# Kernel optimization log

Hardware: AMD Instinct MI355X
Metric: run time of the kernel (lower is better)

The kernel has to match this reference:

```python
import jax, jax.numpy as jnp
import numpy as np


def setup_inputs() -> dict:
    key = jax.random.key(0)
    k1, k2, k3 = jax.random.split(key, 3)
    B, L, C, D, V = 8, 512, 4000, 512, 10000
    x = jax.random.uniform(k1, (B, L, C), dtype=jnp.float32)            # dense char n-gram features
    W_proj = jax.random.normal(k2, (D, C), dtype=jnp.float32) * 0.02     # Linear(char_vsize, d_vec), no bias
    emb_matrix = jax.random.uniform(k3, (V, D), dtype=jnp.float32,
                                    minval=-0.1, maxval=0.1)             # QueryEmb latent embedding table
    return {"x": x, "W_proj": W_proj, "emb_matrix": emb_matrix}


def reference(x, W_proj, emb_matrix):
    # charEmbedder: tanh(Linear(x)) per sentence -> vectorized over batch
    q = jnp.tanh(jnp.einsum('blc,dc->bld', x, W_proj))                   # [B, L, D]
    # QueryEmb: softmax(q @ E^T) @ E + q  (dropout in eval mode = identity)
    attn = jax.nn.softmax(jnp.einsum('bld,vd->blv', q, emb_matrix), axis=-1)  # [B, L, V]
    ctx = jnp.einsum('blv,vd->bld', attn, emb_matrix) + q                # residual
    return ctx
```

## Files before the change

### kernel.cpp

```cpp
#include <hip/hip_runtime.h>
#include <hip/hip_bf16.h>

typedef unsigned short u16;
typedef unsigned int u32;
typedef __bf16 bf16x8 __attribute__((ext_vector_type(8)));
typedef u16 u16x8 __attribute__((ext_vector_type(8)));
typedef float f32x4 __attribute__((ext_vector_type(4)));

#define MM   4096
#define CC   4000
#define KP   4096
#define DD   512
#define VV   10000
#define VPAD 10240

#define WS_Q    0u
#define WS_EB   4194304u
#define WS_ET   14680064u
#define WS_LACC 25165824u
#define WS_P    25182208u
#define OFF_XB  0u
#define OFF_WB  33554432u
#define OFF_QA  37748736u
#define FAST_NEED (WS_P + OFF_QA + 16777216u)
#define WS_PACC 109068288u
#define FULLP_NEED (WS_PACC + 67108864u)

__device__ __forceinline__ u16 f2bf(float f) {
  u32 u = __builtin_bit_cast(u32, f);
  return (u16)((u + 0x7FFFu + ((u >> 16) & 1u)) >> 16);
}
__device__ __forceinline__ float bf2f(u16 h) {
  u32 u = (u32)h << 16;
  return __builtin_bit_cast(float, u);
}

#define GLDS(gp, lp) __builtin_amdgcn_global_load_lds( \
    (const __attribute__((address_space(1))) void*)(gp), \
    (__attribute__((address_space(3))) void*)(lp), 16, 0, 0)

__global__ __launch_bounds__(256) void k_eprep(const float* __restrict__ E,
                                               u16* __restrict__ Eb,
                                               u16* __restrict__ ETb,
                                               float* __restrict__ Out,
                                               float* __restrict__ Lacc) {
  __shared__ u16 st[64 * 65];
  int tid = threadIdx.x;
  {
    int bid = blockIdx.x * 8 + blockIdx.y;
    f32x4 z = {0.f, 0.f, 0.f, 0.f};
    #pragma unroll
    for (int rep = 0; rep < 2; ++rep) {
      int id = bid * 256 + tid + rep * 327680;
      if (id < 524288)      *(f32x4*)(Out + (size_t)id * 4) = z;
      else if (id < 525312) *(f32x4*)(Lacc + (size_t)(id - 524288) * 4) = z;
    }
  }
  int v0 = blockIdx.x * 64, d0 = blockIdx.y * 64;
  int r = tid >> 2, seg = tid & 3;
  u16 h[16];
  int v = v0 + r;
  if (v < VV) {
    const float* src = E + (size_t)v * DD + d0 + seg * 16;
    #pragma unroll
    for (int j = 0; j < 4; ++j) {
      float4 t = *(const float4*)(src + j * 4);
      h[4*j+0] = f2bf(t.x); h[4*j+1] = f2bf(t.y); h[4*j+2] = f2bf(t.z); h[4*j+3] = f2bf(t.w);
    }
  } else {
    #pragma unroll
    for (int j = 0; j < 16; ++j) h[j] = 0;
  }
  {
    u16x8 p0, p1;
    #pragma unroll
    for (int j = 0; j < 8; ++j) { p0[j] = h[j]; p1[j] = h[8+j]; }
    u16* dst = Eb + (size_t)v * DD + d0 + seg * 16;
    *(u16x8*)dst = p0; *(u16x8*)(dst + 8) = p1;
  }
  #pragma unroll
  for (int j = 0; j < 16; ++j) st[r * 65 + seg * 16 + j] = h[j];
  __syncthreads();
  {
    u16 g[16];
    #pragma unroll
    for (int j = 0; j < 16; ++j) g[j] = st[(seg * 16 + j) * 65 + r];
    u16x8 p0, p1;
    #pragma unroll
    for (int j = 0; j < 8; ++j) { p0[j] = g[j]; p1[j] = g[8+j]; }
    u16* dst = ETb + (size_t)(d0 + r) * VPAD + v0 + seg * 16;
    *(u16x8*)dst = p0; *(u16x8*)(dst + 8) = p1;
  }
}

__global__ __launch_bounds__(256) void k_conv(const float* __restrict__ X,
                                              const float* __restrict__ Wp,
                                              u16* __restrict__ Xb,
                                              u16* __restrict__ Wb) {
  int row = blockIdx.x;
  int t = threadIdx.x;
  const float* src;
  u16* dst;
  if (row < MM) { src = X + (size_t)row * CC; dst = Xb + (size_t)row * KP; }
  else { src = Wp + (size_t)(row - MM) * CC; dst = Wb + (size_t)(row - MM) * KP; }
  int c0 = t * 16;
  u16 h[16];
  if (c0 + 16 <= CC) {
    #pragma unroll
    for (int j = 0; j < 4; ++j) {
      float4 v = *(const float4*)(src + c0 + j * 4);
      h[4*j+0] = f2bf(v.x); h[4*j+1] = f2bf(v.y); h[4*j+2] = f2bf(v.z); h[4*j+3] = f2bf(v.w);
    }
  } else {
    #pragma unroll
    for (int j = 0; j < 16; ++j) h[j] = 0;
  }
  u16x8 p0, p1;
  #pragma unroll
  for (int j = 0; j < 8; ++j) { p0[j] = h[j]; p1[j] = h[8+j]; }
  *(u16x8*)(dst + c0) = p0; *(u16x8*)(dst + c0 + 8) = p1;
}

__global__ __launch_bounds__(256) void k_g1(const u16* __restrict__ Xb,
                                            const u16* __restrict__ Wb,
                                            float* __restrict__ Qacc) {
  __shared__ u16 As[128 * 64];
  __shared__ u16 Bs[64 * 64];
  int tid = threadIdx.x;
  int m0 = blockIdx.x * 128;
  int n0 = blockIdx.y * 64;
  int kt0 = blockIdx.z * 32;
  int w = tid >> 6, l = tid & 63;
  int l15 = l & 15, quad = l >> 4;
  int lr = l >> 3, lg = l & 7;
  f32x4 acc[2][4] = {};

  for (int kt = kt0; kt < kt0 + 32; ++kt) {
    #pragma unroll
    for (int i = 0; i < 4; ++i) {
      int wc = i * 4 + w;
      int row = wc * 8 + lr;
      int g = lg ^ (row & 7);
      GLDS(Xb + (size_t)(m0 + row) * KP + kt * 64 + g * 8, As + wc * 512);
      if (i < 2)
        GLDS(Wb + (size_t)(n0 + row) * KP + kt * 64 + g * 8, Bs + wc * 512);
    }
    __syncthreads();
    #pragma unroll
    for (int kk = 0; kk < 2; ++kk) {
      bf16x8 a[2], b[4];
      #pragma unroll
      for (int mi = 0; mi < 2; ++mi) {
        int arow = w * 32 + mi * 16 + l15;
        int slot = (kk * 4 + quad) ^ (arow & 7);
        a[mi] = *(const bf16x8*)&As[arow * 64 + slot * 8];
      }
      #pragma unroll
      for (int ni = 0; ni < 4; ++ni) {
        int brow = ni * 16 + l15;
        int slot = (kk * 4 + quad) ^ (brow & 7);
        b[ni] = *(const bf16x8*)&Bs[brow * 64 + slot * 8];
      }
      #pragma unroll
      for (int mi = 0; mi < 2; ++mi)
        #pragma unroll
        for (int ni = 0; ni < 4; ++ni)
          acc[mi][ni] = __builtin_amdgcn_mfma_f32_16x16x32_bf16(a[mi], b[ni], acc[mi][ni], 0, 0, 0);
    }
    __syncthreads();
  }
  float* dst = Qacc + (size_t)blockIdx.z * (MM * DD);
  #pragma unroll
  for (int mi = 0; mi < 2; ++mi)
    #pragma unroll
    for (int ni = 0; ni < 4; ++ni)
      #pragma unroll
      for (int r = 0; r < 4; ++r) {
        int m = m0 + w * 32 + mi * 16 + quad * 4 + r;
        int d = n0 + ni * 16 + l15;
        dst[(size_t)m * DD + d] = acc[mi][ni][r];
      }
}

__global__ __launch_bounds__(256) void k_tanh(const float* __restrict__ Qacc,
                                              u16* __restrict__ Qb) {
  int idx = blockIdx.x * 256 + threadIdx.x;
  size_t base = (size_t)idx * 8;
  f32x4 a0 = *(const f32x4*)(Qacc + base);
  f32x4 a1 = *(const f32x4*)(Qacc + base + 4);
  f32x4 b0 = *(const f32x4*)(Qacc + (size_t)MM * DD + base);
  f32x4 b1 = *(const f32x4*)(Qacc + (size_t)MM * DD + base + 4);
  u16x8 p;
  #pragma unroll
  for (int j = 0; j < 4; ++j) p[j] = f2bf(tanhf(a0[j] + b0[j]));
  #pragma unroll
  for (int j = 0; j < 4; ++j) p[4 + j] = f2bf(tanhf(a1[j] + b1[j]));
  *(u16x8*)(Qb + base) = p;
}

__global__ __launch_bounds__(256) void k_gemm1(const float* __restrict__ X,
                                               const float* __restrict__ W,
                                               u16* __restrict__ Qb) {
  __shared__ u16 xs[64 * 64];
  __shared__ u16 wst[64 * 64];
  int tid = threadIdx.x;
  int m0 = blockIdx.x * 64;
  int n0 = blockIdx.y * 64;
  int srow = tid >> 2;
  int sseg = tid & 3;
  int r7 = srow & 7;
  const float* xsrc = X + (size_t)(m0 + srow) * CC + sseg * 16;
  const float* wsrc = W + (size_t)(n0 + srow) * CC + sseg * 16;
  int lane = tid & 63;
  int wv = tid >> 6;
  int l15 = lane & 15, quad = lane >> 4;
  f32x4 acc[4] = {};

  for (int kt = 0; kt < 63; ++kt) {
    int cbase = kt * 64 + sseg * 16;
    float xv[16], wf[16];
    if (cbase + 16 <= CC) {
      #pragma unroll
      for (int j = 0; j < 4; ++j) {
        float4 tx = *(const float4*)(xsrc + kt * 64 + j * 4);
        float4 tw = *(const float4*)(wsrc + kt * 64 + j * 4);
        xv[4*j+0] = tx.x; xv[4*j+1] = tx.y; xv[4*j+2] = tx.z; xv[4*j+3] = tx.w;
        wf[4*j+0] = tw.x; wf[4*j+1] = tw.y; wf[4*j+2] = tw.z; wf[4*j+3] = tw.w;
      }
    } else {
      #pragma unroll
      for (int j = 0; j < 16; ++j) { xv[j] = 0.f; wf[j] = 0.f; }
    }
    __syncthreads();
    #pragma unroll
    for (int j = 0; j < 2; ++j) {
      int g = (sseg * 2 + j) ^ r7;
      u16x8 px, pw;
      #pragma unroll
      for (int e = 0; e < 8; ++e) { px[e] = f2bf(xv[8*j+e]); pw[e] = f2bf(wf[8*j+e]); }
      *(u16x8*)&xs[srow * 64 + (g << 3)] = px;
      *(u16x8*)&wst[srow * 64 + (g << 3)] = pw;
    }
    __syncthreads();
    #pragma unroll
    for (int kk = 0; kk < 2; ++kk) {
      int arow = 16 * wv + l15;
      int ga = (kk * 4 + quad) ^ (arow & 7);
      bf16x8 a = *(const bf16x8*)&xs[arow * 64 + (ga << 3)];
      #pragma unroll
      for (int nb = 0; nb < 4; ++nb) {
        int brow = 16 * nb + l15;
        int gb = (kk * 4 + quad) ^ (brow & 7);
        bf16x8 b = *(const bf16x8*)&wst[brow * 64 + (gb << 3)];
        acc[nb] = __builtin_amdgcn_mfma_f32_16x16x32_bf16(a, b, acc[nb], 0, 0, 0);
      }
    }
  }
  #pragma unroll
  for (int nb = 0; nb < 4; ++nb) {
    int d = n0 + 16 * nb + l15;
    #pragma unroll
    for (int r = 0; r < 4; ++r) {
      int m = m0 + 16 * wv + 4 * quad + r;
      Qb[(size_t)m * DD + d] = f2bf(tanhf(acc[nb][r]));
    }
  }
}

__global__ __launch_bounds__(256, 4) void k_s(const u16* __restrict__ Qb,
                                              const u16* __restrict__ Eb,
                                              u16* __restrict__ Pg,
                                              float* __restrict__ Lacc,
                                              int cbase, int W) {
  __shared__ u16 S[16384];
  u16* As = S;
  u16* Bs = S + 8192;
  int tid = threadIdx.x;
  int m0 = blockIdx.x * 128;
  int n0 = blockIdx.y * 128;
  int w = tid >> 6, l = tid & 63;
  int l15 = l & 15, quad = l >> 4;
  int mhalf = w >> 1, nhalf = w & 1;
  int lr = l >> 3, lg = l & 7;
  f32x4 acc[4][4] = {};

  for (int kt = 0; kt < 8; ++kt) {
    #pragma unroll
    for (int i = 0; i < 4; ++i) {
      int wc = i * 4 + w;
      int row = wc * 8 + lr;
      int g = lg ^ (row & 7);
      GLDS(Qb + (size_t)(m0 + row) * DD + kt * 64 + g * 8, As + wc * 512);
      GLDS(Eb + (size_t)(cbase + n0 + row) * DD + kt * 64 + g * 8, Bs + wc * 512);
    }
    __syncthreads();
    #pragma unroll
    for (int kk = 0; kk < 2; ++kk) {
      bf16x8 a[4], b[4];
      #pragma unroll
      for (int mi = 0; mi < 4; ++mi) {
        int arow = mhalf * 64 + mi * 16 + l15;
        int slot = (kk * 4 + quad) ^ (arow & 7);
        a[mi] = *(const bf16x8*)&As[arow * 64 + slot * 8];
      }
      #pragma unroll
      for (int ni = 0; ni < 4; ++ni) {
        int brow = nhalf * 64 + ni * 16 + l15;
        int slot = (kk * 4 + quad) ^ (brow & 7);
        b[ni] = *(const bf16x8*)&Bs[brow * 64 + slot * 8];
      }
      #pragma unroll
      for (int mi = 0; mi < 4; ++mi)
        #pragma unroll
        for (int ni = 0; ni < 4; ++ni)
          acc[mi][ni] = __builtin_amdgcn_mfma_f32_16x16x32_bf16(a[mi], b[ni], acc[mi][ni], 0, 0, 0);
    }
    __syncthreads();
  }

  float rs[4][4] = {};
  #pragma unroll
  for (int mi = 0; mi < 4; ++mi) {
    #pragma unroll
    for (int ni = 0; ni < 4; ++ni) {
      int colL = nhalf * 64 + ni * 16 + l15;
      bool ok = (cbase + n0 + colL) < VV;
      #pragma unroll
      for (int r = 0; r < 4; ++r) {
        int rowL = mhalf * 64 + mi * 16 + quad * 4 + r;
        float p = ok ? __expf(acc[mi][ni][r]) : 0.f;
        rs[mi][r] += p;
        S[rowL * 128 + (((colL >> 3) ^ (rowL & 15)) << 3) + (colL & 7)] = f2bf(p);
      }
    }
  }
  __syncthreads();
  {
    int row = tid >> 1, h2 = tid & 1;
    size_t gbase = (size_t)(m0 + row) * W + n0 + h2 * 64;
    #pragma unroll
    for (int g = 0; g < 8; ++g) {
      int pg = (h2 * 8 + g) ^ (row & 15);
      u16x8 v = *(const u16x8*)&S[row * 128 + pg * 8];
      *(u16x8*)(Pg + gbase + g * 8) = v;
    }
  }
  #pragma unroll
  for (int mi = 0; mi < 4; ++mi)
    #pragma unroll
    for (int r = 0; r < 4; ++r) {
      float v = rs[mi][r];
      v += __shfl_xor(v, 1, 16);
      v += __shfl_xor(v, 2, 16);
      v += __shfl_xor(v, 4, 16);
      v += __shfl_xor(v, 8, 16);
      if (l15 == 0)
        atomicAdd(&Lacc[m0 + mhalf * 64 + mi * 16 + quad * 4 + r], v);
    }
}

__global__ __launch_bounds__(256, 4) void k_pvs(const u16* __restrict__ Pg,
                                                const u16* __restrict__ ETb,
                                                float* __restrict__ Pacc) {
  __shared__ u16 S[16384];
  u16* As = S;
  u16* Bs = S + 8192;
  int tid = threadIdx.x;
  int m0 = blockIdx.x * 128;
  int d0 = blockIdx.y * 128;
  int z = blockIdx.z;
  int w = tid >> 6, l = tid & 63;
  int l15 = l & 15, quad = l >> 4;
  int mhalf = w >> 1, nhalf = w & 1;
  int lr = l >> 3, lg = l & 7;
  f32x4 acc[4][4] = {};
  int kt0 = z * 20;

  for (int kt = kt0; kt < kt0 + 20; ++kt) {
    #pragma unroll
    for (int i = 0; i < 4; ++i) {
      int wc = i * 4 + w;
      int row = wc * 8 + lr;
      int g = lg ^ (row & 7);
      GLDS(Pg + (size_t)(m0 + row) * VPAD + kt * 64 + g * 8, As + wc * 512);
      GLDS(ETb + (size_t)(d0 + row) * VPAD + kt * 64 + g * 8, Bs + wc * 512);
    }
    __syncthreads();
    #pragma unroll
    for (int kk = 0; kk < 2; ++kk) {
      bf16x8 a[4], b[4];
      #pragma unroll
      for (int mi = 0; mi < 4; ++mi) {
        int arow = mhalf * 64 + mi * 16 + l15;
        int slot = (kk * 4 + quad) ^ (arow & 7);
        a[mi] = *(const bf16x8*)&As[arow * 64 + slot * 8];
      }
      #pragma unroll
      for (int ni = 0; ni < 4; ++ni) {
        int brow = nhalf * 64 + ni * 16 + l15;
        int slot = (kk * 4 + quad) ^ (brow & 7);
        b[ni] = *(const bf16x8*)&Bs[brow * 64 + slot * 8];
      }
      #pragma unroll
      for (int mi = 0; mi < 4; ++mi)
        #pragma unroll
        for (int ni = 0; ni < 4; ++ni)
          acc[mi][ni] = __builtin_amdgcn_mfma_f32_16x16x32_bf16(a[mi], b[ni], acc[mi][ni], 0, 0, 0);
    }
    __syncthreads();
  }
  float* dst = Pacc + (size_t)z * (MM * DD);
  #pragma unroll
  for (int mi = 0; mi < 4; ++mi)
    #pragma unroll
    for (int ni = 0; ni < 4; ++ni)
      #pragma unroll
      for (int r = 0; r < 4; ++r) {
        int m = m0 + mhalf * 64 + mi * 16 + quad * 4 + r;
        int d = d0 + nhalf * 64 + ni * 16 + l15;
        dst[(size_t)m * DD + d] = acc[mi][ni][r];
      }
}

__global__ __launch_bounds__(256) void k_pv(const u16* __restrict__ Pg,
                                            const u16* __restrict__ ETb,
                                            float* __restrict__ Out,
                                            int cbase, int W) {
  __shared__ u16 As[128 * 64];
  __shared__ u16 Bs[64 * 64];
  int tid = threadIdx.x;
  int m0 = blockIdx.x * 128;
  int n0 = blockIdx.y * 64;
  int w = tid >> 6, l = tid & 63;
  int l15 = l & 15, quad = l >> 4;
  int lr = l >> 3, lg = l & 7;
  int iters = W >> 6;
  f32x4 acc[2][4] = {};

  for (int kt = 0; kt < iters; ++kt) {
    #pragma unroll
    for (int i = 0; i < 4; ++i) {
      int wc = i * 4 + w;
      int row = wc * 8 + lr;
      int g = lg ^ (row & 7);
      GLDS(Pg + (size_t)(m0 + row) * W + kt * 64 + g * 8, As + wc * 512);
      if (i < 2)
        GLDS(ETb + (size_t)(n0 + row) * VPAD + cbase + kt * 64 + g * 8, Bs + wc * 512);
    }
    __syncthreads();
    #pragma unroll
    for (int kk = 0; kk < 2; ++kk) {
      bf16x8 a[2], b[4];
      #pragma unroll
      for (int mi = 0; mi < 2; ++mi) {
        int arow = w * 32 + mi * 16 + l15;
        int slot = (kk * 4 + quad) ^ (arow & 7);
        a[mi] = *(const bf16x8*)&As[arow * 64 + slot * 8];
      }
      #pragma unroll
      for (int ni = 0; ni < 4; ++ni) {
        int brow = ni * 16 + l15;
        int slot = (kk * 4 + quad) ^ (brow & 7);
        b[ni] = *(const bf16x8*)&Bs[brow * 64 + slot * 8];
      }
      #pragma unroll
      for (int mi = 0; mi < 2; ++mi)
        #pragma unroll
        for (int ni = 0; ni < 4; ++ni)
          acc[mi][ni] = __builtin_amdgcn_mfma_f32_16x16x32_bf16(a[mi], b[ni], acc[mi][ni], 0, 0, 0);
    }
    __syncthreads();
  }
  #pragma unroll
  for (int mi = 0; mi < 2; ++mi)
    #pragma unroll
    for (int ni = 0; ni < 4; ++ni)
      #pragma unroll
      for (int r = 0; r < 4; ++r) {
        int m = m0 + w * 32 + mi * 16 + quad * 4 + r;
        int d = n0 + ni * 16 + l15;
        Out[(size_t)m * DD + d] += acc[mi][ni][r];
      }
}

__global__ __launch_bounds__(256) void k_fin8(float* __restrict__ Out,
                                              const float* __restrict__ Lacc,
                                              const u16* __restrict__ Qb,
                                              const float* __restrict__ Pacc) {
  int idx = blockIdx.x * 256 + threadIdx.x;
  int m = idx >> 7;
  int d4 = (idx & 127) * 4;
  float inv = 1.f / Lacc[m];
  size_t off = (size_t)m * DD + d4;
  f32x4 s = {0.f, 0.f, 0.f, 0.f};
  #pragma unroll
  for (int z = 0; z < 8; ++z)
    s += *(const f32x4*)(Pacc + (size_t)z * (MM * DD) + off);
  const u16* qp = Qb + off;
  f32x4 r;
  #pragma unroll
  for (int i = 0; i < 4; ++i) r[i] = s[i] * inv + bf2f(qp[i]);
  *(f32x4*)(Out + off) = r;
}

__global__ __launch_bounds__(256) void k_fin(float* __restrict__ Out,
                                             const float* __restrict__ Lacc,
                                             const u16* __restrict__ Qb) {
  int idx = blockIdx.x * 256 + threadIdx.x;
  int m = idx >> 7;
  int d4 = (idx & 127) * 4;
  float inv = 1.f / Lacc[m];
  f32x4 ov = *(const f32x4*)(Out + (size_t)m * DD + d4);
  const u16* qp = Qb + (size_t)m * DD + d4;
  f32x4 r;
  #pragma unroll
  for (int i = 0; i < 4; ++i) r[i] = ov[i] * inv + bf2f(qp[i]);
  *(f32x4*)(Out + (size_t)m * DD + d4) = r;
}

extern "C" void kernel_launch(void* const* d_in, const int* in_sizes, int n_in,
                              void* d_out, int out_size, void* d_ws, size_t ws_size,
                              hipStream_t stream) {
  const float* x  = (const float*)d_in[0];
  const float* Wp = (const float*)d_in[1];
  const float* E  = (const float*)d_in[2];
  float* out = (float*)d_out;
  char* ws = (char*)d_ws;
  u16*   Qb   = (u16*)(ws + WS_Q);
  u16*   Eb   = (u16*)(ws + WS_EB);
  u16*   ETb  = (u16*)(ws + WS_ET);
  float* Lacc = (float*)(ws + WS_LACC);
  u16*   Pc   = (u16*)(ws + WS_P);
  u16*   Xb   = (u16*)(ws + WS_P + OFF_XB);
  u16*   Wb   = (u16*)(ws + WS_P + OFF_WB);
  float* Qacc = (float*)(ws + WS_P + OFF_QA);
  float* Pacc = (float*)(ws + WS_PACC);

  bool fastg = ws_size >= (size_t)FAST_NEED;
  bool fullp = ws_size >= (size_t)FULLP_NEED;

  k_eprep<<<dim3(VPAD / 64, DD / 64), 256, 0, stream>>>(E, Eb, ETb, out, Lacc);
  if (fastg) {
    k_conv<<<dim3(MM + DD), 256, 0, stream>>>(x, Wp, Xb, Wb);
    k_g1<<<dim3(MM / 128, DD / 64, 2), 256, 0, stream>>>(Xb, Wb, Qacc);
    k_tanh<<<dim3(MM * DD / 8 / 256), 256, 0, stream>>>(Qacc, Qb);
  } else {
    k_gemm1<<<dim3(MM / 64, DD / 64), 256, 0, stream>>>(x, Wp, Qb);
  }
  if (fullp) {
    k_s  <<<dim3(MM / 128, VPAD / 128), 256, 0, stream>>>(Qb, Eb, Pc, Lacc, 0, VPAD);
    k_pvs<<<dim3(MM / 128, DD / 128, 8), 256, 0, stream>>>(Pc, ETb, Pacc);
    k_fin8<<<dim3(MM * DD / 4 / 256), 256, 0, stream>>>(out, Lacc, Qb, Pacc);
  } else {
    int W = 640;
    if (ws_size >= (size_t)WS_P + (size_t)MM * 2560 * 2) W = 2560;
    else if (ws_size >= (size_t)WS_P + (size_t)MM * 1280 * 2) W = 1280;
    int nch = VPAD / W;
    for (int c = 0; c < nch; ++c) {
      k_s <<<dim3(MM / 128, W / 128), 256, 0, stream>>>(Qb, Eb, Pc, Lacc, c * W, W);
      k_pv<<<dim3(MM / 128, DD / 64), 256, 0, stream>>>(Pc, ETb, out, c * W, W);
    }
    k_fin<<<dim3(MM * DD / 4 / 256), 256, 0, stream>>>(out, Lacc, Qb);
  }
}
```

Before: 297.8 us.

## Switch attention GEMMs to FP8 with scaled operands and rebalance split-K

Quantizes the embedding table, its transpose, tanh(q) and the softmax probabilities to FP8 (E4M3-like, with power-of-two prescales) and runs both attention GEMMs on fp8 MFMA instructions. The goal is to halve operand bytes and use the higher fp8 matrix throughput. The projection GEMM moves to 4-way split-K and the PV GEMM to 4-way split, with new tanh and finalize kernels to match. In exchange it loses precision, clamps logits before exp, drops the output zeroing, and adds a workspace-size-gated path.

```diff
diff --git a/kernel.cpp b/kernel.cpp
--- a/kernel.cpp
+++ b/kernel.cpp
@@ -3,9 +3,11 @@
 
 typedef unsigned short u16;
 typedef unsigned int u32;
+typedef unsigned char u8;
 typedef __bf16 bf16x8 __attribute__((ext_vector_type(8)));
 typedef u16 u16x8 __attribute__((ext_vector_type(8)));
 typedef float f32x4 __attribute__((ext_vector_type(4)));
+typedef u32 u32x4 __attribute__((ext_vector_type(4)));
 
 #define MM   4096
 #define CC   4000
@@ -14,17 +16,23 @@
 #define VV   10000
 #define VPAD 10240
 
+#define WS8_QB   0u
+#define WS8_QF   4194304u
+#define WS8_EF   6291456u
+#define WS8_ETF  11534336u
+#define WS8_LACC 16777216u
+#define WS8_R    16793600u
+#define R_XB     0u
+#define R_WB     33554432u
+#define R_QA     37748736u
+#define WS8_PACC 88096768u
+#define FAST8_NEED 121651200u
+
 #define WS_Q    0u
 #define WS_EB   4194304u
 #define WS_ET   14680064u
 #define WS_LACC 25165824u
 #define WS_P    25182208u
-#define OFF_XB  0u
-#define OFF_WB  33554432u
-#define OFF_QA  37748736u
-#define FAST_NEED (WS_P + OFF_QA + 16777216u)
-#define WS_PACC 109068288u
-#define FULLP_NEED (WS_PACC + 67108864u)
 
 __device__ __forceinline__ u16 f2bf(float f) {
   u32 u = __builtin_bit_cast(u32, f);
@@ -34,62 +42,70 @@
   u32 u = (u32)h << 16;
   return __builtin_bit_cast(float, u);
 }
+__device__ __forceinline__ u8 f2fp8(float f) {
+  u32 u = __builtin_bit_cast(u32, f);
+  u32 s = (u >> 31) << 7;
+  u32 m = u & 0x7FFFFFFFu;
+  if (m < 0x3C800000u) return (u8)s;
+  u32 r = m + 0x7FFFFu + ((m >> 20) & 1u);
+  return (u8)(((r >> 20) - 960u) | s);
+}
 
 #define GLDS(gp, lp) __builtin_amdgcn_global_load_lds( \
     (const __attribute__((address_space(1))) void*)(gp), \
     (__attribute__((address_space(3))) void*)(lp), 16, 0, 0)
 
-__global__ __launch_bounds__(256) void k_eprep(const float* __restrict__ E,
-                                               u16* __restrict__ Eb,
-                                               u16* __restrict__ ETb,
-                                               float* __restrict__ Out,
-                                               float* __restrict__ Lacc) {
-  __shared__ u16 st[64 * 65];
+__device__ __forceinline__ int fo8(int row, int o) {
+  return row * 64 + ((((o >> 1) ^ ((row >> 1) & 3)) << 4) | ((o & 1) << 3));
+}
+
+
+__global__ __launch_bounds__(256) void k_eprep8(const float* __restrict__ E,
+                                                u8* __restrict__ Ef,
+                                                u8* __restrict__ ETf,
+                                                float* __restrict__ Lacc) {
+  __shared__ u8 st[64 * 68];
   int tid = threadIdx.x;
   {
-    int bid = blockIdx.x * 8 + blockIdx.y;
-    f32x4 z = {0.f, 0.f, 0.f, 0.f};
-    #pragma unroll
-    for (int rep = 0; rep < 2; ++rep) {
-      int id = bid * 256 + tid + rep * 327680;
-      if (id < 524288)      *(f32x4*)(Out + (size_t)id * 4) = z;
-      else if (id < 525312) *(f32x4*)(Lacc + (size_t)(id - 524288) * 4) = z;
-    }
+    int flat = blockIdx.x * 8 + blockIdx.y;
+    int fid = flat * 256 + tid;
+    if (fid < MM) Lacc[fid] = 0.f;
   }
   int v0 = blockIdx.x * 64, d0 = blockIdx.y * 64;
   int r = tid >> 2, seg = tid & 3;
-  u16 h[16];
+  u8 h[16];
   int v = v0 + r;
   if (v < VV) {
     const float* src = E + (size_t)v * DD + d0 + seg * 16;
     #pragma unroll
     for (int j = 0; j < 4; ++j) {
       float4 t = *(const float4*)(src + j * 4);
-      h[4*j+0] = f2bf(t.x); h[4*j+1] = f2bf(t.y); h[4*j+2] = f2bf(t.z); h[4*j+3] = f2bf(t.w);
+      h[4*j+0] = f2fp8(t.x * 16.f); h[4*j+1] = f2fp8(t.y * 16.f);
+      h[4*j+2] = f2fp8(t.z * 16.f); h[4*j+3] = f2fp8(t.w * 16.f);
     }
   } else {
     #pragma unroll
     for (int j = 0; j < 16; ++j) h[j] = 0;
   }
   {
-    u16x8 p0, p1;
-    #pragma unroll
-    for (int j = 0; j < 8; ++j) { p0[j] = h[j]; p1[j] = h[8+j]; }
-    u16* dst = Eb + (size_t)v * DD + d0 + seg * 16;
-    *(u16x8*)dst = p0; *(u16x8*)(dst + 8) = p1;
-  }
-  #pragma unroll
-  for (int j = 0; j < 16; ++j) st[r * 65 + seg * 16 + j] = h[j];
+    u32x4 p;
+    #pragma unroll
+    for (int q = 0; q < 4; ++q)
+      p[q] = (u32)h[4*q] | ((u32)h[4*q+1] << 8) | ((u32)h[4*q+2] << 16) | ((u32)h[4*q+3] << 24);
+    *(u32x4*)(Ef + (size_t)v * DD + d0 + seg * 16) = p;
+  }
+  #pragma unroll
+  for (int j = 0; j < 16; ++j) st[r * 68 + seg * 16 + j] = h[j];
   __syncthreads();
   {
-    u16 g[16];
-    #pragma unroll
-    for (int j = 0; j < 16; ++j) g[j] = st[(seg * 16 + j) * 65 + r];
-    u16x8 p0, p1;
-    #pragma unroll
-    for (int j = 0; j < 8; ++j) { p0[j] = g[j]; p1[j] = g[8+j]; }
-    u16* dst = ETb + (size_t)(d0 + r) * VPAD + v0 + seg * 16;
-    *(u16x8*)dst = p0; *(u16x8*)(dst + 8) = p1;
+    u8 g[16];
+    #pragma unroll
+    for (int j = 0; j < 16; ++j) g[j] = st[(seg * 16 + j) * 68 + r];
+    u32x4 p;
+    #pragma unroll
+    for (int q = 0; q < 4; ++q)
+      p[q] = (u32)g[4*q] | ((u32)g[4*q+1] << 8) | ((u32)g[4*q+2] << 16) | ((u32)g[4*q+3] << 24);
+    *(u32x4*)(ETf + (size_t)(d0 + r) * VPAD + v0 + seg * 16) = p;
   }
 }
 
@@ -129,13 +145,13 @@
   int tid = threadIdx.x;
   int m0 = blockIdx.x * 128;
   int n0 = blockIdx.y * 64;
-  int kt0 = blockIdx.z * 32;
+  int kt0 = blockIdx.z * 16;
   int w = tid >> 6, l = tid & 63;
   int l15 = l & 15, quad = l >> 4;
   int lr = l >> 3, lg = l & 7;
   f32x4 acc[2][4] = {};
 
-  for (int kt = kt0; kt < kt0 + 32; ++kt) {
+  for (int kt = kt0; kt < kt0 + 16; ++kt) {
     #pragma unroll
     for (int i = 0; i < 4; ++i) {
       int wc = i * 4 + w;
@@ -182,20 +198,258 @@
       }
 }
 
-__global__ __launch_bounds__(256) void k_tanh(const float* __restrict__ Qacc,
-                                              u16* __restrict__ Qb) {
+__global__ __launch_bounds__(256) void k_tanh4(const float* __restrict__ Qacc,
+                                               u16* __restrict__ Qb,
+                                               u8* __restrict__ Qf) {
   int idx = blockIdx.x * 256 + threadIdx.x;
   size_t base = (size_t)idx * 8;
-  f32x4 a0 = *(const f32x4*)(Qacc + base);
-  f32x4 a1 = *(const f32x4*)(Qacc + base + 4);
-  f32x4 b0 = *(const f32x4*)(Qacc + (size_t)MM * DD + base);
-  f32x4 b1 = *(const f32x4*)(Qacc + (size_t)MM * DD + base + 4);
+  f32x4 s0 = {0,0,0,0}, s1 = {0,0,0,0};
+  #pragma unroll
+  for (int z = 0; z < 4; ++z) {
+    s0 += *(const f32x4*)(Qacc + (size_t)z * (MM * DD) + base);
+    s1 += *(const f32x4*)(Qacc + (size_t)z * (MM * DD) + base + 4);
+  }
+  float t[8];
+  #pragma unroll
+  for (int j = 0; j < 4; ++j) t[j] = tanhf(s0[j]);
+  #pragma unroll
+  for (int j = 0; j < 4; ++j) t[4+j] = tanhf(s1[j]);
   u16x8 p;
   #pragma unroll
-  for (int j = 0; j < 4; ++j) p[j] = f2bf(tanhf(a0[j] + b0[j]));
-  #pragma unroll
-  for (int j = 0; j < 4; ++j) p[4 + j] = f2bf(tanhf(a1[j] + b1[j]));
+  for (int j = 0; j < 8; ++j) p[j] = f2bf(t[j]);
   *(u16x8*)(Qb + base) = p;
+  unsigned long long q8 = 0;
+  #pragma unroll
+  for (int j = 0; j < 8; ++j) q8 |= ((unsigned long long)f2fp8(t[j] * 4.f)) << (8 * j);
+  *(unsigned long long*)(Qf + base) = q8;
+}
+
+__global__ __launch_bounds__(256, 4) void k_s8(const u8* __restrict__ Qf,
+                                               const u8* __restrict__ Ef,
+                                               u8* __restrict__ Pf,
+                                               float* __restrict__ Lacc) {
+  __shared__ u8 S8[16384];
+  u8* As = S8;
+  u8* Bs = S8 + 8192;
+  int tid = threadIdx.x;
+  int m0 = blockIdx.x * 128;
+  int n0 = blockIdx.y * 128;
+  int w = tid >> 6, l = tid & 63;
+  int l15 = l & 15, quad = l >> 4;
+  int mhalf = w >> 1, nhalf = w & 1;
+  int srow = tid >> 2, schunk = tid & 3;
+  int sw0 = schunk ^ ((srow >> 1) & 3);
+  int sw1 = schunk ^ (((srow + 64) >> 1) & 3);
+  const u8* qa0 = Qf + (size_t)(m0 + srow) * DD + sw0 * 16;
+  const u8* qa1 = Qf + (size_t)(m0 + 64 + srow) * DD + sw1 * 16;
+  const u8* eb0 = Ef + (size_t)(n0 + srow) * DD + sw0 * 16;
+  const u8* eb1 = Ef + (size_t)(n0 + 64 + srow) * DD + sw1 * 16;
+  f32x4 acc[4][4] = {};
+
+  for (int kt = 0; kt < 8; ++kt) {
+    GLDS(qa0 + kt * 64, As + tid * 16);
+    GLDS(qa1 + kt * 64, As + 4096 + tid * 16);
+    GLDS(eb0 + kt * 64, Bs + tid * 16);
+    GLDS(eb1 + kt * 64, Bs + 4096 + tid * 16);
+    __syncthreads();
+    #pragma unroll
+    for (int kk = 0; kk < 2; ++kk) {
+      long a[4], b[4];
+      #pragma unroll
+      for (int mi = 0; mi < 4; ++mi) {
+        int arow = mhalf * 64 + mi * 16 + l15;
+        a[mi] = *(const long*)&As[fo8(arow, kk * 4 + quad)];
+      }
+      #pragma unroll
+      for (int ni = 0; ni < 4; ++ni) {
+        int brow = nhalf * 64 + ni * 16 + l15;
+        b[ni] = *(const long*)&Bs[fo8(brow, kk * 4 + quad)];
+      }
+      #pragma unroll
+      for (int mi = 0; mi < 4; ++mi)
+        #pragma unroll
+        for (int ni = 0; ni < 4; ++ni)
+          acc[mi][ni] = __builtin_amdgcn_mfma_f32_16x16x32_fp8_fp8(a[mi], b[ni], acc[mi][ni], 0, 0, 0);
+    }
+    __syncthreads();
+  }
+
+  float rs[4][4] = {};
+  #pragma unroll
+  for (int mi = 0; mi < 4; ++mi) {
+    #pragma unroll
+    for (int ni = 0; ni < 4; ++ni) {
+      int colL = nhalf * 64 + ni * 16 + l15;
+      bool ok = (n0 + colL) < VV;
+      #pragma unroll
+      for (int r = 0; r < 4; ++r) {
+        int rowL = mhalf * 64 + mi * 16 + quad * 4 + r;
+        float p = ok ? __expf(fminf(acc[mi][ni][r] * 0.015625f, 5.9f)) : 0.f;
+        rs[mi][r] += p;
+        S8[rowL * 128 + (((colL >> 4) ^ (rowL & 7)) << 4) + (colL & 15)] = f2fp8(p * 0.25f);
+      }
+    }
+  }
+  __syncthreads();
+  {
+    int row = tid >> 1, h2 = tid & 1;
+    size_t gbase = (size_t)(m0 + row) * VPAD + n0 + h2 * 64;
+    #pragma unroll
+    for (int c = 0; c < 4; ++c) {
+      int slot = (h2 * 4 + c) ^ (row & 7);
+      *(u32x4*)(Pf + gbase + c * 16) = *(const u32x4*)&S8[row * 128 + slot * 16];
+    }
+  }
+  #pragma unroll
+  for (int mi = 0; mi < 4; ++mi)
+    #pragma unroll
+    for (int r = 0; r < 4; ++r) {
+      float v = rs[mi][r];
+      v += __shfl_xor(v, 1, 16);
+      v += __shfl_xor(v, 2, 16);
+      v += __shfl_xor(v, 4, 16);
+      v += __shfl_xor(v, 8, 16);
+      if (l15 == 0)
+        atomicAdd(&Lacc[m0 + mhalf * 64 + mi * 16 + quad * 4 + r], v);
+    }
+}
+
+__global__ __launch_bounds__(256, 4) void k_pvs8(const u8* __restrict__ Pf,
+                                                 const u8* __restrict__ ETf,
+                                                 float* __restrict__ Pacc) {
+  __shared__ u8 S8[16384];
+  u8* As = S8;
+  u8* Bs = S8 + 8192;
+  int tid = threadIdx.x;
+  int m0 = blockIdx.x * 128;
+  int d0 = blockIdx.y * 128;
+  int z = blockIdx.z;
+  int w = tid >> 6, l = tid & 63;
+  int l15 = l & 15, quad = l >> 4;
+  int mhalf = w >> 1, nhalf = w & 1;
+  int srow = tid >> 2, schunk = tid & 3;
+  int sw0 = schunk ^ ((srow >> 1) & 3);
+  int sw1 = schunk ^ (((srow + 64) >> 1) & 3);
+  const u8* pa0 = Pf + (size_t)(m0 + srow) * VPAD + sw0 * 16;
+  const u8* pa1 = Pf + (size_t)(m0 + 64 + srow) * VPAD + sw1 * 16;
+  const u8* eb0 = ETf + (size_t)(d0 + srow) * VPAD + sw0 * 16;
+  const u8* eb1 = ETf + (size_t)(d0 + 64 + srow) * VPAD + sw1 * 16;
+  f32x4 acc[4][4] = {};
+  int kt0 = z * 40;
+
+  for (int kt = kt0; kt < kt0 + 40; ++kt) {
+    GLDS(pa0 + kt * 64, As + tid * 16);
+    GLDS(pa1 + kt * 64, As + 4096 + tid * 16);
+    GLDS(eb0 + kt * 64, Bs + tid * 16);
+    GLDS(eb1 + kt * 64, Bs + 4096 + tid * 16);
+    __syncthreads();
+    #pragma unroll
+    for (int kk = 0; kk < 2; ++kk) {
+      long a[4], b[4];
+      #pragma unroll
+      for (int mi = 0; mi < 4; ++mi) {
+        int arow = mhalf * 64 + mi * 16 + l15;
+        a[mi] = *(const long*)&As[fo8(arow, kk * 4 + quad)];
+      }
+      #pragma unroll
+      for (int ni = 0; ni < 4; ++ni) {
+        int brow = nhalf * 64 + ni * 16 + l15;
+        b[ni] = *(const long*)&Bs[fo8(brow, kk * 4 + quad)];
+      }
+      #pragma unroll
+      for (int mi = 0; mi < 4; ++mi)
+        #pragma unroll
+        for (int ni = 0; ni < 4; ++ni)
+          acc[mi][ni] = __builtin_amdgcn_mfma_f32_16x16x32_fp8_fp8(a[mi], b[ni], acc[mi][ni], 0, 0, 0);
+    }
+    __syncthreads();
+  }
+  float* dst = Pacc + (size_t)z * (MM * DD);
+  #pragma unroll
+  for (int mi = 0; mi < 4; ++mi)
+    #pragma unroll
+    for (int ni = 0; ni < 4; ++ni)
+      #pragma unroll
+      for (int r = 0; r < 4; ++r) {
+        int m = m0 + mhalf * 64 + mi * 16 + quad * 4 + r;
+        int d = d0 + nhalf * 64 + ni * 16 + l15;
+        dst[(size_t)m * DD + d] = acc[mi][ni][r];
+      }
+}
+
+__global__ __launch_bounds__(256) void k_fin4(float* __restrict__ Out,
+                                              const float* __restrict__ Lacc,
+                                              const u16* __restrict__ Qb,
+                                              const float* __restrict__ Pacc) {
+  int idx = blockIdx.x * 256 + threadIdx.x;
+  int m = idx >> 7;
+  int d4 = (idx & 127) * 4;
+  float inv = 0.25f / Lacc[m];
+  size_t off = (size_t)m * DD + d4;
+  f32x4 s = {0.f, 0.f, 0.f, 0.f};
+  #pragma unroll
+  for (int z = 0; z < 4; ++z)
+    s += *(const f32x4*)(Pacc + (size_t)z * (MM * DD) + off);
+  const u16* qp = Qb + off;
+  f32x4 r;
+  #pragma unroll
+  for (int i = 0; i < 4; ++i) r[i] = s[i] * inv + bf2f(qp[i]);
+  *(f32x4*)(Out + off) = r;
+}
+
+
+__global__ __launch_bounds__(256) void k_eprep(const float* __restrict__ E,
+                                               u16* __restrict__ Eb,
+                                               u16* __restrict__ ETb,
+                                               float* __restrict__ Out,
+                                               float* __restrict__ Lacc) {
+  __shared__ u16 st[64 * 65];
+  int tid = threadIdx.x;
+  {
+    int bid = blockIdx.x * 8 + blockIdx.y;
+    f32x4 z = {0.f, 0.f, 0.f, 0.f};
+    #pragma unroll
+    for (int rep = 0; rep < 2; ++rep) {
+      int id = bid * 256 + tid + rep * 327680;
+      if (id < 524288)      *(f32x4*)(Out + (size_t)id * 4) = z;
+      else if (id < 525312) *(f32x4*)(Lacc + (size_t)(id - 524288) * 4) = z;
+    }
+  }
+  int v0 = blockIdx.x * 64, d0 = blockIdx.y * 64;
+  int r = tid >> 2, seg = tid & 3;
+  u16 h[16];
+  int v = v0 + r;
+  if (v < VV) {
+    const float* src = E + (size_t)v * DD + d0 + seg * 16;
+    #pragma unroll
+    for (int j = 0; j < 4; ++j) {
+      float4 t = *(const float4*)(src + j * 4);
+      h[4*j+0] = f2bf(t.x); h[4*j+1] = f2bf(t.y); h[4*j+2] = f2bf(t.z); h[4*j+3] = f2bf(t.w);
+    }
+  } else {
+    #pragma unroll
+    for (int j = 0; j < 16; ++j) h[j] = 0;
+  }
+  {
+    u16x8 p0, p1;
+    #pragma unroll
+    for (int j = 0; j < 8; ++j) { p0[j] = h[j]; p1[j] = h[8+j]; }
+    u16* dst = Eb + (size_t)v * DD + d0 + seg * 16;
+    *(u16x8*)dst = p0; *(u16x8*)(dst + 8) = p1;
+  }
+  #pragma unroll
+  for (int j = 0; j < 16; ++j) st[r * 65 + seg * 16 + j] = h[j];
+  __syncthreads();
+  {
+    u16 g[16];
+    #pragma unroll
+    for (int j = 0; j < 16; ++j) g[j] = st[(seg * 16 + j) * 65 + r];
+    u16x8 p0, p1;
+    #pragma unroll
+    for (int j = 0; j < 8; ++j) { p0[j] = g[j]; p1[j] = g[8+j]; }
+    u16* dst = ETb + (size_t)(d0 + r) * VPAD + v0 + seg * 16;
+    *(u16x8*)dst = p0; *(u16x8*)(dst + 8) = p1;
+  }
 }
 
 __global__ __launch_bounds__(256) void k_gemm1(const float* __restrict__ X,
@@ -267,14 +521,13 @@
   }
 }
 
-__global__ __launch_bounds__(256, 4) void k_s(const u16* __restrict__ Qb,
-                                              const u16* __restrict__ Eb,
-                                              u16* __restrict__ Pg,
-                                              float* __restrict__ Lacc,
-                                              int cbase, int W) {
-  __shared__ u16 S[16384];
-  u16* As = S;
-  u16* Bs = S + 8192;
+__global__ __launch_bounds__(256) void k_s(const u16* __restrict__ Qb,
+                                           const u16* __restrict__ Eb,
+                                           u16* __restrict__ Pg,
+                                           float* __restrict__ Lacc,
+                                           int cbase, int W) {
+  __shared__ u16 As[128 * 64];
+  __shared__ u16 Bs[128 * 64];
   int tid = threadIdx.x;
   int m0 = blockIdx.x * 128;
   int n0 = blockIdx.y * 128;
@@ -323,26 +576,15 @@
   for (int mi = 0; mi < 4; ++mi) {
     #pragma unroll
     for (int ni = 0; ni < 4; ++ni) {
-      int colL = nhalf * 64 + ni * 16 + l15;
-      bool ok = (cbase + n0 + colL) < VV;
+      int ncol = n0 + nhalf * 64 + ni * 16 + l15;
+      bool ok = (cbase + ncol) < VV;
       #pragma unroll
       for (int r = 0; r < 4; ++r) {
-        int rowL = mhalf * 64 + mi * 16 + quad * 4 + r;
         float p = ok ? __expf(acc[mi][ni][r]) : 0.f;
         rs[mi][r] += p;
-        S[rowL * 128 + (((colL >> 3) ^ (rowL & 15)) << 3) + (colL & 7)] = f2bf(p);
-      }
-    }
-  }
-  __syncthreads();
-  {
-    int row = tid >> 1, h2 = tid & 1;
-    size_t gbase = (size_t)(m0 + row) * W + n0 + h2 * 64;
-    #pragma unroll
-    for (int g = 0; g < 8; ++g) {
-      int pg = (h2 * 8 + g) ^ (row & 15);
-      u16x8 v = *(const u16x8*)&S[row * 128 + pg * 8];
-      *(u16x8*)(Pg + gbase + g * 8) = v;
+        int m = m0 + mhalf * 64 + mi * 16 + quad * 4 + r;
+        Pg[(size_t)m * W + ncol] = f2bf(p);
+      }
     }
   }
   #pragma unroll
@@ -357,69 +599,6 @@
       if (l15 == 0)
         atomicAdd(&Lacc[m0 + mhalf * 64 + mi * 16 + quad * 4 + r], v);
     }
-}
-
-__global__ __launch_bounds__(256, 4) void k_pvs(const u16* __restrict__ Pg,
-                                                const u16* __restrict__ ETb,
-                                                float* __restrict__ Pacc) {
-  __shared__ u16 S[16384];
-  u16* As = S;
-  u16* Bs = S + 8192;
-  int tid = threadIdx.x;
-  int m0 = blockIdx.x * 128;
-  int d0 = blockIdx.y * 128;
-  int z = blockIdx.z;
-  int w = tid >> 6, l = tid & 63;
-  int l15 = l & 15, quad = l >> 4;
-  int mhalf = w >> 1, nhalf = w & 1;
-  int lr = l >> 3, lg = l & 7;
-  f32x4 acc[4][4] = {};
-  int kt0 = z * 20;
-
-  for (int kt = kt0; kt < kt0 + 20; ++kt) {
-    #pragma unroll
-    for (int i = 0; i < 4; ++i) {
-      int wc = i * 4 + w;
-      int row = wc * 8 + lr;
-      int g = lg ^ (row & 7);
-      GLDS(Pg + (size_t)(m0 + row) * VPAD + kt * 64 + g * 8, As + wc * 512);
-      GLDS(ETb + (size_t)(d0 + row) * VPAD + kt * 64 + g * 8, Bs + wc * 512);
-    }
-    __syncthreads();
-    #pragma unroll
-    for (int kk = 0; kk < 2; ++kk) {
-      bf16x8 a[4], b[4];
-      #pragma unroll
-      for (int mi = 0; mi < 4; ++mi) {
-        int arow = mhalf * 64 + mi * 16 + l15;
-        int slot = (kk * 4 + quad) ^ (arow & 7);
-        a[mi] = *(const bf16x8*)&As[arow * 64 + slot * 8];
-      }
-      #pragma unroll
-      for (int ni = 0; ni < 4; ++ni) {
-        int brow = nhalf * 64 + ni * 16 + l15;
-        int slot = (kk * 4 + quad) ^ (brow & 7);
-        b[ni] = *(const bf16x8*)&Bs[brow * 64 + slot * 8];
-      }
-      #pragma unroll
-      for (int mi = 0; mi < 4; ++mi)
-        #pragma unroll
-        for (int ni = 0; ni < 4; ++ni)
-          acc[mi][ni] = __builtin_amdgcn_mfma_f32_16x16x32_bf16(a[mi], b[ni], acc[mi][ni], 0, 0, 0);
-    }
-    __syncthreads();
-  }
-  float* dst = Pacc + (size_t)z * (MM * DD);
-  #pragma unroll
-  for (int mi = 0; mi < 4; ++mi)
-    #pragma unroll
-    for (int ni = 0; ni < 4; ++ni)
-      #pragma unroll
-      for (int r = 0; r < 4; ++r) {
-        int m = m0 + mhalf * 64 + mi * 16 + quad * 4 + r;
-        int d = d0 + nhalf * 64 + ni * 16 + l15;
-        dst[(size_t)m * DD + d] = acc[mi][ni][r];
-      }
 }
 
 __global__ __launch_bounds__(256) void k_pv(const u16* __restrict__ Pg,
@@ -483,26 +662,6 @@
       }
 }
 
-__global__ __launch_bounds__(256) void k_fin8(float* __restrict__ Out,
-                                              const float* __restrict__ Lacc,
-                                              const u16* __restrict__ Qb,
-                                              const float* __restrict__ Pacc) {
-  int idx = blockIdx.x * 256 + threadIdx.x;
-  int m = idx >> 7;
-  int d4 = (idx & 127) * 4;
-  float inv = 1.f / Lacc[m];
-  size_t off = (size_t)m * DD + d4;
-  f32x4 s = {0.f, 0.f, 0.f, 0.f};
-  #pragma unroll
-  for (int z = 0; z < 8; ++z)
-    s += *(const f32x4*)(Pacc + (size_t)z * (MM * DD) + off);
-  const u16* qp = Qb + off;
-  f32x4 r;
-  #pragma unroll
-  for (int i = 0; i < 4; ++i) r[i] = s[i] * inv + bf2f(qp[i]);
-  *(f32x4*)(Out + off) = r;
-}
-
 __global__ __launch_bounds__(256) void k_fin(float* __restrict__ Out,
                                              const float* __restrict__ Lacc,
                                              const u16* __restrict__ Qb) {
@@ -526,36 +685,38 @@
   const float* E  = (const float*)d_in[2];
   float* out = (float*)d_out;
   char* ws = (char*)d_ws;
-  u16*   Qb   = (u16*)(ws + WS_Q);
-  u16*   Eb   = (u16*)(ws + WS_EB);
-  u16*   ETb  = (u16*)(ws + WS_ET);
-  float* Lacc = (float*)(ws + WS_LACC);
-  u16*   Pc   = (u16*)(ws + WS_P);
-  u16*   Xb   = (u16*)(ws + WS_P + OFF_XB);
-  u16*   Wb   = (u16*)(ws + WS_P + OFF_WB);
-  float* Qacc = (float*)(ws + WS_P + OFF_QA);
-  float* Pacc = (float*)(ws + WS_PACC);
-
-  bool fastg = ws_size >= (size_t)FAST_NEED;
-  bool fullp = ws_size >= (size_t)FULLP_NEED;
-
-  k_eprep<<<dim3(VPAD / 64, DD / 64), 256, 0, stream>>>(E, Eb, ETb, out, Lacc);
-  if (fastg) {
+
+  if (ws_size >= (size_t)FAST8_NEED) {
+    u16*   Qb   = (u16*)(ws + WS8_QB);
+    u8*    Qf   = (u8*)(ws + WS8_QF);
+    u8*    Ef   = (u8*)(ws + WS8_EF);
+    u8*    ETf  = (u8*)(ws + WS8_ETF);
+    float* Lacc = (float*)(ws + WS8_LACC);
+    u16*   Xb   = (u16*)(ws + WS8_R + R_XB);
+    u16*   Wb   = (u16*)(ws + WS8_R + R_WB);
+    float* Qacc = (float*)(ws + WS8_R + R_QA);
+    u8*    Pf   = (u8*)(ws + WS8_R);
+    float* Pacc = (float*)(ws + WS8_PACC);
+
+    k_eprep8<<<dim3(VPAD / 64, DD / 64), 256, 0, stream>>>(E, Ef, ETf, Lacc);
     k_conv<<<dim3(MM + DD), 256, 0, stream>>>(x, Wp, Xb, Wb);
-    k_g1<<<dim3(MM / 128, DD / 64, 2), 256, 0, stream>>>(Xb, Wb, Qacc);
-    k_tanh<<<dim3(MM * DD / 8 / 256), 256, 0, stream>>>(Qacc, Qb);
+    k_g1<<<dim3(MM / 128, DD / 64, 4), 256, 0, stream>>>(Xb, Wb, Qacc);
+    k_tanh4<<<dim3(MM * DD / 8 / 256), 256, 0, stream>>>(Qacc, Qb, Qf);
+    k_s8<<<dim3(MM / 128, VPAD / 128), 256, 0, stream>>>(Qf, Ef, Pf, Lacc);
+    k_pvs8<<<dim3(MM / 128, DD / 128, 4), 256, 0, stream>>>(Pf, ETf, Pacc);
+    k_fin4<<<dim3(MM * DD / 4 / 256), 256, 0, stream>>>(out, Lacc, Qb, Pacc);
   } else {
-    k_gemm1<<<dim3(MM / 64, DD / 64), 256, 0, stream>>>(x, Wp, Qb);
-  }
-  if (fullp) {
-    k_s  <<<dim3(MM / 128, VPAD / 128), 256, 0, stream>>>(Qb, Eb, Pc, Lacc, 0, VPAD);
-    k_pvs<<<dim3(MM / 128, DD / 128, 8), 256, 0, stream>>>(Pc, ETb, Pacc);
-    k_fin8<<<dim3(MM * DD / 4 / 256), 256, 0, stream>>>(out, Lacc, Qb, Pacc);
-  } else {
+    u16*   Qb   = (u16*)(ws + WS_Q);
+    u16*   Eb   = (u16*)(ws + WS_EB);
+    u16*   ETb  = (u16*)(ws + WS_ET);
+    float* Lacc = (float*)(ws + WS_LACC);
+    u16*   Pc   = (u16*)(ws + WS_P);
     int W = 640;
     if (ws_size >= (size_t)WS_P + (size_t)MM * 2560 * 2) W = 2560;
     else if (ws_size >= (size_t)WS_P + (size_t)MM * 1280 * 2) W = 1280;
     int nch = VPAD / W;
+    k_eprep<<<dim3(VPAD / 64, DD / 64), 256, 0, stream>>>(E, Eb, ETb, out, Lacc);
+    k_gemm1<<<dim3(MM / 64, DD / 64), 256, 0, stream>>>(x, Wp, Qb);
     for (int c = 0; c < nch; ++c) {
       k_s <<<dim3(MM / 128, W / 128), 256, 0, stream>>>(Qb, Eb, Pc, Lacc, c * W, W);
       k_pv<<<dim3(MM / 128, DD / 64), 256, 0, stream>>>(Pc, ETb, out, c * W, W);
```

After: 272.8 us. -8.4%, faster.
